# Optimization experiments

Measured on AMD Instinct MI355X. Metric: run time of the kernel, lower is better.

## Reference

```python
import jax, jax.numpy as jnp
import numpy as np

DIM = 256
NH = 8
HD = DIM // NH          # 32
KD = HD // 2            # 16, attn_ratio=0.5
SCALE = KD ** -0.5
EPS = 1e-3              # BatchNorm2d eps=0.001
B, H, W = 8, 32, 32


def _bn(x, g, b, m, v):
    # inference-mode BatchNorm2d over channel axis 1 of NCHW
    inv = g / jnp.sqrt(v + EPS)
    return x * inv[None, :, None, None] + (b - m * inv)[None, :, None, None]


def setup_inputs() -> dict:
    key = jax.random.key(0)
    ks = jax.random.split(key, 16)
    h_out = DIM + 2 * NH * KD  # 512
    return {
        "x": jax.random.normal(ks[0], (B, DIM, H, W), jnp.float32),
        "qkv_w": jax.random.normal(ks[1], (h_out, DIM), jnp.float32) * 0.05,
        "qkv_g": jax.random.uniform(ks[2], (h_out,), jnp.float32, 0.5, 1.5),
        "qkv_b": jax.random.normal(ks[3], (h_out,), jnp.float32) * 0.1,
        "qkv_m": jax.random.normal(ks[4], (h_out,), jnp.float32) * 0.1,
        "qkv_v": jax.random.uniform(ks[5], (h_out,), jnp.float32, 0.5, 1.5),
        "pe_w": jax.random.normal(ks[6], (DIM, 1, 3, 3), jnp.float32) * 0.1,
        "pe_g": jax.random.uniform(ks[7], (DIM,), jnp.float32, 0.5, 1.5),
        "pe_b": jax.random.normal(ks[8], (DIM,), jnp.float32) * 0.1,
        "pe_m": jax.random.normal(ks[9], (DIM,), jnp.float32) * 0.1,
        "pe_v": jax.random.uniform(ks[10], (DIM,), jnp.float32, 0.5, 1.5),
        "proj_w": jax.random.normal(ks[11], (DIM, DIM), jnp.float32) * 0.05,
        "proj_g": jax.random.uniform(ks[12], (DIM,), jnp.float32, 0.5, 1.5),
        "proj_b": jax.random.normal(ks[13], (DIM,), jnp.float32) * 0.1,
        "proj_m": jax.random.normal(ks[14], (DIM,), jnp.float32) * 0.1,
        "proj_v": jax.random.uniform(ks[15], (DIM,), jnp.float32, 0.5, 1.5),
    }


def reference(x, qkv_w, qkv_g, qkv_b, qkv_m, qkv_v,
              pe_w, pe_g, pe_b, pe_m, pe_v,
              proj_w, proj_g, proj_b, proj_m, proj_v):
    b, c, h, w = x.shape
    n = h * w
    # qkv: 1x1 conv (no bias) + BN, act=Identity
    qkv = _bn(jnp.einsum('oc,bchw->bohw', qkv_w, x), qkv_g, qkv_b, qkv_m, qkv_v)
    qkv = qkv.reshape(b, NH, 2 * KD + HD, n)
    q, k, v = jnp.split(qkv, [KD, 2 * KD], axis=2)  # [b,nh,kd,n],[b,nh,kd,n],[b,nh,hd,n]
    # attn = q^T @ k * scale, softmax over keys (last dim)
    attn = jax.nn.softmax(jnp.einsum('bhkn,bhkm->bhnm', q, k) * SCALE, axis=-1)
    # v @ attn^T -> [b,nh,hd,n]
    out = jnp.einsum('bhdj,bhij->bhdi', v, attn).reshape(b, c, h, w)
    # depthwise 3x3 positional branch on v (reshaped to spatial)
    v_sp = v.reshape(b, c, h, w)
    pe = jax.lax.conv_general_dilated(v_sp, pe_w, window_strides=(1, 1),
                                      padding=((1, 1), (1, 1)),
                                      feature_group_count=c)
    pe = _bn(pe, pe_g, pe_b, pe_m, pe_v)
    x_attn = out + pe
    # final 1x1 projection + BN
    return _bn(jnp.einsum('oc,bchw->bohw', proj_w, x_attn),
               proj_g, proj_b, proj_m, proj_v)
```

## Files before the change

### kernel.cpp

```cpp
#include <hip/hip_runtime.h>
#include <hip/hip_bf16.h>

#define B_    8
#define DIM_  256
#define NH_   8
#define HD_   32
#define KD_   16
#define HOUT_ 512
#define N_    1024
#define SCALE_ 0.25f
#define EPS_  1e-3f

typedef unsigned short u16;
typedef unsigned int   u32;
typedef __attribute__((ext_vector_type(8)))  short short8;
typedef __attribute__((ext_vector_type(4)))  float f32x4;
typedef __attribute__((ext_vector_type(16))) float f32x16;

union H4 { uint2 u; u16 e[4]; };
union FragU { uint4 u; short8 s; };
union F8 { short8 s; u16 e[8]; };

__device__ __forceinline__ float b2f(u16 u) {
    union { unsigned int i; float f; } c;
    c.i = ((unsigned int)u) << 16;
    return c.f;
}

__device__ __forceinline__ u16 f2b(float f) {
    union { float f; unsigned int i; } c;
    c.f = f;
    unsigned int x = c.i;
    return (u16)((x + 0x7fffu + ((x >> 16) & 1u)) >> 16);
}

__device__ __forceinline__ short8 cvt8(const float* p) {
    float4 a = ((const float4*)p)[0];
    float4 b = ((const float4*)p)[1];
    F8 f;
    f.e[0] = f2b(a.x); f.e[1] = f2b(a.y); f.e[2] = f2b(a.z); f.e[3] = f2b(a.w);
    f.e[4] = f2b(b.x); f.e[5] = f2b(b.y); f.e[6] = f2b(b.z); f.e[7] = f2b(b.w);
    return f.s;
}

__global__ __launch_bounds__(256) void k_qkv(
    const float* __restrict__ x, const float* __restrict__ qw,
    const float* __restrict__ qg, const float* __restrict__ qb,
    const float* __restrict__ qm, const float* __restrict__ qv,
    u16* __restrict__ qkv)
{
    __shared__ u16 x_s[128][40];
    __shared__ float2 bn_s[64];
    int blk = blockIdx.x;
    int nb = blk & 7, ob = (blk >> 3) & 7, b = blk >> 6;
    int t = threadIdx.x;
    int wv_ = t >> 6, lane = t & 63, quad = lane >> 4, l16 = lane & 15;
    int o_base = ob * 64 + (wv_ & 1) * 32;
    int nw = (wv_ >> 1) * 64;

    if (t < 64) {
        int o = ob * 64 + t;
        float inv  = qg[o] / sqrtf(qv[o] + EPS_);
        float beta = qb[o] - qm[o] * inv;
        if (t < 16) { inv *= SCALE_; beta *= SCALE_; }
        bn_s[t] = make_float2(inv, beta);
    }

    f32x4 acc[2][4];
    #pragma unroll
    for (int ot = 0; ot < 2; ++ot)
        #pragma unroll
        for (int nt = 0; nt < 4; ++nt) acc[ot][nt] = (f32x4){0.f, 0.f, 0.f, 0.f};

    const float* xb = x + (size_t)b * DIM_ * N_ + nb * 128;
    int sn = t & 127;
    int sc = (t >> 7) * 16;

    for (int c0 = 0; c0 < DIM_; c0 += 32) {
        short8 af[2];
        #pragma unroll
        for (int ot = 0; ot < 2; ++ot)
            af[ot] = cvt8(qw + (size_t)(o_base + ot * 16 + l16) * DIM_ + c0 + quad * 8);
        __syncthreads();
        {
            u16 tmp[16];
            #pragma unroll
            for (int j = 0; j < 16; ++j)
                tmp[j] = f2b(xb[(size_t)(c0 + sc + j) * N_ + sn]);
            *(uint4*)&x_s[sn][sc]     = *(uint4*)&tmp[0];
            *(uint4*)&x_s[sn][sc + 8] = *(uint4*)&tmp[8];
        }
        __syncthreads();
        short8 bf[4];
        #pragma unroll
        for (int nt = 0; nt < 4; ++nt)
            bf[nt] = *(const short8*)&x_s[nw + nt * 16 + l16][quad * 8];
        #pragma unroll
        for (int ot = 0; ot < 2; ++ot)
            #pragma unroll
            for (int nt = 0; nt < 4; ++nt)
                acc[ot][nt] = __builtin_amdgcn_mfma_f32_16x16x32_bf16(af[ot], bf[nt], acc[ot][nt], 0, 0, 0);
    }
    #pragma unroll
    for (int ot = 0; ot < 2; ++ot)
        #pragma unroll
        for (int r = 0; r < 4; ++r) {
            int ol = (wv_ & 1) * 32 + ot * 16 + quad * 4 + r;
            float2 ib = bn_s[ol];
            u16* dst = qkv + (size_t)(b * HOUT_ + ob * 64 + ol) * N_ + nb * 128 + nw + l16;
            #pragma unroll
            for (int nt = 0; nt < 4; ++nt)
                dst[nt * 16] = f2b(acc[ot][nt][r] * ib.x + ib.y);
        }
}

struct MainS { u16 q_t[64][24]; u16 k_t[2][256][24]; };
struct EpiS  { u16 o_acc[2][32][66]; float l_s[2][64]; float v_pe[128][33]; };
union  SmemU { MainS m; EpiS e; };

__global__ __launch_bounds__(256, 4) void k_attn(
    const u16* __restrict__ qkv, const float* __restrict__ pew,
    const float* __restrict__ eg, const float* __restrict__ eb,
    const float* __restrict__ em, const float* __restrict__ ev,
    u16* __restrict__ xattnT)
{
    __shared__ SmemU su;
    __shared__ float wpe_s[32][10];
    int blk = blockIdx.x;
    int qb = blk & 15;
    int h  = (blk >> 4) & 7;
    int b  = blk >> 7;
    int t    = threadIdx.x;
    int wv_  = t >> 6;
    int lane = t & 63;
    int q5   = lane & 31;
    int hw   = lane >> 5;
    int kh   = wv_ >> 1;
    int qt   = wv_ & 1;
    const u16* base = qkv + (size_t)(b * HOUT_ + h * 64) * N_;
    int q0g = qb * 64;

    if (t < 32) {
        int c = h * 32 + t;
        float inv = eg[c] / sqrtf(ev[c] + EPS_);
        #pragma unroll
        for (int k = 0; k < 9; ++k) wpe_s[t][k] = pew[c * 9 + k] * inv;
        wpe_s[t][9] = eb[c] - em[c] * inv;
    }
    {
        int q = t & 63, d4 = (t >> 6) * 4;
        H4 hh;
        #pragma unroll
        for (int i = 0; i < 4; ++i)
            hh.e[i] = base[(size_t)(d4 + i) * N_ + q0g + q];
        *(uint2*)&su.m.q_t[q][d4] = hh.u;
    }
    __syncthreads();

    short8 qf = *(const short8*)&su.m.q_t[qt * 32 + q5][hw * 8];

    f32x16 oacc = {0.f,0.f,0.f,0.f, 0.f,0.f,0.f,0.f, 0.f,0.f,0.f,0.f, 0.f,0.f,0.f,0.f};
    float l_lane = 0.f;

    for (int ch = 0; ch < 2; ++ch) {
        __syncthreads();
        {
            #pragma unroll
            for (int s2 = 0; s2 < 2; ++s2) {
                int key = s2 * 512 + ch * 256 + t;
                #pragma unroll
                for (int d4 = 0; d4 < 16; d4 += 4) {
                    H4 hh;
                    #pragma unroll
                    for (int i = 0; i < 4; ++i)
                        hh.e[i] = base[(size_t)(16 + d4 + i) * N_ + key];
                    *(uint2*)&su.m.k_t[s2][t][d4] = hh.u;
                }
            }
        }
        __syncthreads();

        #pragma unroll 2
        for (int tile = 0; tile < 8; ++tile) {
            int key0 = kh * 512 + ch * 256 + tile * 32;
            short8 kf = *(const short8*)&su.m.k_t[kh][tile * 32 + q5][hw * 8];
            f32x16 z = {0.f,0.f,0.f,0.f, 0.f,0.f,0.f,0.f, 0.f,0.f,0.f,0.f, 0.f,0.f,0.f,0.f};
            f32x16 sT = __builtin_amdgcn_mfma_f32_32x32x16_bf16(kf, qf, z, 0, 0, 0);
            u32 pk[8];
            #pragma unroll
            for (int j = 0; j < 8; ++j) {
                float p0 = __expf(fminf(sT[2 * j], 80.f));
                float p1 = __expf(fminf(sT[2 * j + 1], 80.f));
                l_lane += p0 + p1;
                pk[j] = (u32)f2b(p0) | ((u32)f2b(p1) << 16);
            }
            #pragma unroll
            for (int s = 0; s < 2; ++s) {
                u32 s0 = hw ? pk[4 * s + 0] : pk[4 * s + 2];
                u32 s1 = hw ? pk[4 * s + 1] : pk[4 * s + 3];
                u32 r0 = __shfl_xor(s0, 32);
                u32 r1 = __shfl_xor(s1, 32);
                FragU pf;
                pf.u.x = hw ? r0 : pk[4 * s + 0];
                pf.u.y = hw ? r1 : pk[4 * s + 1];
                pf.u.z = hw ? pk[4 * s + 2] : r0;
                pf.u.w = hw ? pk[4 * s + 3] : r1;
                const u16* vsrc = base + (size_t)(32 + q5) * N_ + key0 + s * 16 + hw * 8;
                short8 vf = *(const short8*)vsrc;
                oacc = __builtin_amdgcn_mfma_f32_32x32x16_bf16(vf, pf.s, oacc, 0, 0, 0);
            }
        }
    }

    float l_q = l_lane + __shfl_xor(l_lane, 32);
    __syncthreads();

    {
        int qg = qt * 32 + q5;
        #pragma unroll
        for (int r = 0; r < 16; ++r) {
            int d = (r & 3) + 8 * (r >> 2) + 4 * hw;
            su.e.o_acc[kh][d][qg] = f2b(oacc[r]);
        }
        if (hw == 0) su.e.l_s[kh][qg] = l_q;
    }
    {
        int ybase = qb * 2 - 1;
        #pragma unroll
        for (int i = 0; i < 16; ++i) {
            int idx = i * 256 + t;
            int d = idx >> 7, px = idx & 127;
            int y = ybase + (px >> 5);
            float v = 0.f;
            if (y >= 0 && y < 32)
                v = b2f(base[(size_t)(32 + d) * N_ + y * 32 + (px & 31)]);
            su.e.v_pe[px][d] = v;
        }
    }
    __syncthreads();

    {
        int d = t & 31, pxg = t >> 5;
        float w9[9];
        #pragma unroll
        for (int k = 0; k < 9; ++k) w9[k] = wpe_s[d][k];
        float beta = wpe_s[d][9];
        int c = h * 32 + d;
        #pragma unroll
        for (int ii = 0; ii < 8; ++ii) {
            int pl = pxg * 8 + ii;
            int xx0 = pl & 31;
            float s = beta;
            #pragma unroll
            for (int dy = -1; dy <= 1; ++dy) {
                #pragma unroll
                for (int dx = -1; dx <= 1; ++dx) {
                    int xx = xx0 + dx;
                    if (xx < 0 || xx > 31) continue;
                    s += w9[(dy + 1) * 3 + (dx + 1)] * su.e.v_pe[pl + 32 + dy * 32 + dx][d];
                }
            }
            float o = b2f(su.e.o_acc[0][d][pl]) + b2f(su.e.o_acc[1][d][pl]);
            float l = su.e.l_s[0][pl] + su.e.l_s[1][pl];
            xattnT[(size_t)(b * N_ + q0g + pl) * DIM_ + c] = f2b(o / fmaxf(l, 1e-30f) + s);
        }
    }
}

__global__ __launch_bounds__(256) void k_proj(
    const u16* __restrict__ xattnT, const float* __restrict__ pw,
    const float* __restrict__ pg, const float* __restrict__ pb,
    const float* __restrict__ pm, const float* __restrict__ pv,
    float* __restrict__ out)
{
    __shared__ float2 bn_s[64];
    int blk = blockIdx.x;
    int nb = blk & 15, ob = (blk >> 4) & 3, b = blk >> 6;
    int t = threadIdx.x;
    int wv_ = t >> 6, lane = t & 63, quad = lane >> 4, l16 = lane & 15;
    int o_base = ob * 64 + (wv_ & 1) * 32;
    int n_base = nb * 64 + (wv_ >> 1) * 32;

    if (t < 64) {
        int o = ob * 64 + t;
        float inv = pg[o] / sqrtf(pv[o] + EPS_);
        bn_s[t] = make_float2(inv, pb[o] - pm[o] * inv);
    }
    __syncthreads();

    f32x4 acc[2][2];
    #pragma unroll
    for (int ot = 0; ot < 2; ++ot)
        #pragma unroll
        for (int nt = 0; nt < 2; ++nt) acc[ot][nt] = (f32x4){0.f, 0.f, 0.f, 0.f};

    const u16* xb = xattnT + (size_t)b * N_ * DIM_;
    for (int c0 = 0; c0 < DIM_; c0 += 32) {
        short8 af[2];
        #pragma unroll
        for (int ot = 0; ot < 2; ++ot)
            af[ot] = cvt8(pw + (size_t)(o_base + ot * 16 + l16) * DIM_ + c0 + quad * 8);
        short8 bf[2];
        #pragma unroll
        for (int nt = 0; nt < 2; ++nt)
            bf[nt] = *(const short8*)(xb + (size_t)(n_base + nt * 16 + l16) * DIM_ + c0 + quad * 8);
        #pragma unroll
        for (int ot = 0; ot < 2; ++ot)
            #pragma unroll
            for (int nt = 0; nt < 2; ++nt)
                acc[ot][nt] = __builtin_amdgcn_mfma_f32_16x16x32_bf16(af[ot], bf[nt], acc[ot][nt], 0, 0, 0);
    }
    #pragma unroll
    for (int ot = 0; ot < 2; ++ot)
        #pragma unroll
        for (int r = 0; r < 4; ++r) {
            int ol = (wv_ & 1) * 32 + ot * 16 + quad * 4 + r;
            float2 ib = bn_s[ol];
            float* dst = out + (size_t)(b * DIM_ + ob * 64 + ol) * N_ + n_base + l16;
            #pragma unroll
            for (int nt = 0; nt < 2; ++nt)
                dst[nt * 16] = acc[ot][nt][r] * ib.x + ib.y;
        }
}

extern "C" void kernel_launch(void* const* d_in, const int* in_sizes, int n_in,
                              void* d_out, int out_size, void* d_ws, size_t ws_size,
                              hipStream_t stream)
{
    const float* x      = (const float*)d_in[0];
    const float* qkv_w  = (const float*)d_in[1];
    const float* qkv_g  = (const float*)d_in[2];
    const float* qkv_b  = (const float*)d_in[3];
    const float* qkv_m  = (const float*)d_in[4];
    const float* qkv_v  = (const float*)d_in[5];
    const float* pe_w   = (const float*)d_in[6];
    const float* pe_g   = (const float*)d_in[7];
    const float* pe_b   = (const float*)d_in[8];
    const float* pe_m   = (const float*)d_in[9];
    const float* pe_v   = (const float*)d_in[10];
    const float* proj_w = (const float*)d_in[11];
    const float* proj_g = (const float*)d_in[12];
    const float* proj_b = (const float*)d_in[13];
    const float* proj_m = (const float*)d_in[14];
    const float* proj_v = (const float*)d_in[15];
    float* out = (float*)d_out;

    char* p = (char*)d_ws;
    u16* qkv    = (u16*)p;  p += (size_t)B_ * HOUT_ * N_ * sizeof(u16);
    u16* xattnT = (u16*)p;

    hipLaunchKernelGGL(k_qkv, dim3(512), dim3(256), 0, stream,
                       x, qkv_w, qkv_g, qkv_b, qkv_m, qkv_v, qkv);
    hipLaunchKernelGGL(k_attn, dim3(1024), dim3(256), 0, stream,
                       qkv, pe_w, pe_g, pe_b, pe_m, pe_v, xattnT);
    hipLaunchKernelGGL(k_proj, dim3(512), dim3(256), 0, stream,
                       xattnT, proj_w, proj_g, proj_b, proj_m, proj_v, out);
}
```

Measured before the change: 146.8 us.

## Give each attention wave all keys for its own query tile, halving the grid

Each attention block now handles 128 queries, and each of its four waves processes all 1024 keys for its own 32 queries. Before, waves split the keys in half and the two partial results were merged through shared memory. The full K for the head is staged once into shared memory, split into lo/hi halves with padded rows, so the per-chunk reload and extra barriers go away. The 1/l normalisation is applied in registers before the epilogue. Risks: half as many blocks (512), a larger shared-memory footprint, and the occupancy hint removed, which may lower occupancy and latency hiding.

```diff
diff --git a/kernel.cpp b/kernel.cpp
--- a/kernel.cpp
+++ b/kernel.cpp
@@ -20,6 +20,7 @@
 union H4 { uint2 u; u16 e[4]; };
 union FragU { uint4 u; short8 s; };
 union F8 { short8 s; u16 e[8]; };
+union F8u { uint2 u2[2]; short8 s; };
 
 __device__ __forceinline__ float b2f(u16 u) {
     union { unsigned int i; float f; } c;
@@ -114,11 +115,11 @@
         }
 }
 
-struct MainS { u16 q_t[64][24]; u16 k_t[2][256][24]; };
-struct EpiS  { u16 o_acc[2][32][66]; float l_s[2][64]; float v_pe[128][33]; };
+struct MainS { u16 q_lo[128][10]; u16 q_hi[128][10]; u16 k_lo[1024][10]; u16 k_hi[1024][10]; };
+struct EpiS  { float v_pe[192][33]; u16 o_s[4][32][34]; };
 union  SmemU { MainS m; EpiS e; };
 
-__global__ __launch_bounds__(256, 4) void k_attn(
+__global__ __launch_bounds__(256) void k_attn(
     const u16* __restrict__ qkv, const float* __restrict__ pew,
     const float* __restrict__ eg, const float* __restrict__ eb,
     const float* __restrict__ em, const float* __restrict__ ev,
@@ -127,18 +128,16 @@
     __shared__ SmemU su;
     __shared__ float wpe_s[32][10];
     int blk = blockIdx.x;
-    int qb = blk & 15;
-    int h  = (blk >> 4) & 7;
-    int b  = blk >> 7;
+    int qb = blk & 7;
+    int h  = (blk >> 3) & 7;
+    int b  = blk >> 6;
     int t    = threadIdx.x;
     int wv_  = t >> 6;
     int lane = t & 63;
     int q5   = lane & 31;
     int hw   = lane >> 5;
-    int kh   = wv_ >> 1;
-    int qt   = wv_ & 1;
     const u16* base = qkv + (size_t)(b * HOUT_ + h * 64) * N_;
-    int q0g = qb * 64;
+    int q0g = qb * 128;
 
     if (t < 32) {
         int c = h * 32 + t;
@@ -148,93 +147,102 @@
         wpe_s[t][9] = eb[c] - em[c] * inv;
     }
     {
-        int q = t & 63, d4 = (t >> 6) * 4;
-        H4 hh;
-        #pragma unroll
-        for (int i = 0; i < 4; ++i)
-            hh.e[i] = base[(size_t)(d4 + i) * N_ + q0g + q];
-        *(uint2*)&su.m.q_t[q][d4] = hh.u;
+        int q = t & 127, half = t >> 7;
+        u16 tmp[8];
+        #pragma unroll
+        for (int j = 0; j < 8; ++j)
+            tmp[j] = base[(size_t)(half * 8 + j) * N_ + q0g + q];
+        u16 (*dst)[10] = half ? su.m.q_hi : su.m.q_lo;
+        *(uint2*)&dst[q][0] = *(uint2*)&tmp[0];
+        *(uint2*)&dst[q][4] = *(uint2*)&tmp[4];
+    }
+    {
+        #pragma unroll
+        for (int s = 0; s < 4; ++s) {
+            int key = s * 256 + t;
+            u16 tmp[16];
+            #pragma unroll
+            for (int d = 0; d < 16; ++d)
+                tmp[d] = base[(size_t)(16 + d) * N_ + key];
+            *(uint2*)&su.m.k_lo[key][0] = *(uint2*)&tmp[0];
+            *(uint2*)&su.m.k_lo[key][4] = *(uint2*)&tmp[4];
+            *(uint2*)&su.m.k_hi[key][0] = *(uint2*)&tmp[8];
+            *(uint2*)&su.m.k_hi[key][4] = *(uint2*)&tmp[12];
+        }
     }
     __syncthreads();
 
-    short8 qf = *(const short8*)&su.m.q_t[qt * 32 + q5][hw * 8];
+    const u16 (*qarr)[10] = hw ? su.m.q_hi : su.m.q_lo;
+    const u16 (*karr)[10] = hw ? su.m.k_hi : su.m.k_lo;
+    short8 qf;
+    {
+        F8u f;
+        f.u2[0] = *(const uint2*)&qarr[wv_ * 32 + q5][0];
+        f.u2[1] = *(const uint2*)&qarr[wv_ * 32 + q5][4];
+        qf = f.s;
+    }
 
     f32x16 oacc = {0.f,0.f,0.f,0.f, 0.f,0.f,0.f,0.f, 0.f,0.f,0.f,0.f, 0.f,0.f,0.f,0.f};
     float l_lane = 0.f;
 
-    for (int ch = 0; ch < 2; ++ch) {
-        __syncthreads();
-        {
-            #pragma unroll
-            for (int s2 = 0; s2 < 2; ++s2) {
-                int key = s2 * 512 + ch * 256 + t;
-                #pragma unroll
-                for (int d4 = 0; d4 < 16; d4 += 4) {
-                    H4 hh;
-                    #pragma unroll
-                    for (int i = 0; i < 4; ++i)
-                        hh.e[i] = base[(size_t)(16 + d4 + i) * N_ + key];
-                    *(uint2*)&su.m.k_t[s2][t][d4] = hh.u;
-                }
-            }
-        }
-        __syncthreads();
-
-        #pragma unroll 2
-        for (int tile = 0; tile < 8; ++tile) {
-            int key0 = kh * 512 + ch * 256 + tile * 32;
-            short8 kf = *(const short8*)&su.m.k_t[kh][tile * 32 + q5][hw * 8];
-            f32x16 z = {0.f,0.f,0.f,0.f, 0.f,0.f,0.f,0.f, 0.f,0.f,0.f,0.f, 0.f,0.f,0.f,0.f};
-            f32x16 sT = __builtin_amdgcn_mfma_f32_32x32x16_bf16(kf, qf, z, 0, 0, 0);
-            u32 pk[8];
-            #pragma unroll
-            for (int j = 0; j < 8; ++j) {
-                float p0 = __expf(fminf(sT[2 * j], 80.f));
-                float p1 = __expf(fminf(sT[2 * j + 1], 80.f));
-                l_lane += p0 + p1;
-                pk[j] = (u32)f2b(p0) | ((u32)f2b(p1) << 16);
-            }
-            #pragma unroll
-            for (int s = 0; s < 2; ++s) {
-                u32 s0 = hw ? pk[4 * s + 0] : pk[4 * s + 2];
-                u32 s1 = hw ? pk[4 * s + 1] : pk[4 * s + 3];
-                u32 r0 = __shfl_xor(s0, 32);
-                u32 r1 = __shfl_xor(s1, 32);
-                FragU pf;
-                pf.u.x = hw ? r0 : pk[4 * s + 0];
-                pf.u.y = hw ? r1 : pk[4 * s + 1];
-                pf.u.z = hw ? pk[4 * s + 2] : r0;
-                pf.u.w = hw ? pk[4 * s + 3] : r1;
-                const u16* vsrc = base + (size_t)(32 + q5) * N_ + key0 + s * 16 + hw * 8;
-                short8 vf = *(const short8*)vsrc;
-                oacc = __builtin_amdgcn_mfma_f32_32x32x16_bf16(vf, pf.s, oacc, 0, 0, 0);
-            }
+    #pragma unroll 4
+    for (int tile = 0; tile < 32; ++tile) {
+        int key0 = tile * 32;
+        F8u kfu;
+        kfu.u2[0] = *(const uint2*)&karr[key0 + q5][0];
+        kfu.u2[1] = *(const uint2*)&karr[key0 + q5][4];
+        f32x16 z = {0.f,0.f,0.f,0.f, 0.f,0.f,0.f,0.f, 0.f,0.f,0.f,0.f, 0.f,0.f,0.f,0.f};
+        f32x16 sT = __builtin_amdgcn_mfma_f32_32x32x16_bf16(kfu.s, qf, z, 0, 0, 0);
+        u32 pk[8];
+        #pragma unroll
+        for (int j = 0; j < 8; ++j) {
+            float p0 = __expf(fminf(sT[2 * j], 80.f));
+            float p1 = __expf(fminf(sT[2 * j + 1], 80.f));
+            l_lane += p0 + p1;
+            pk[j] = (u32)f2b(p0) | ((u32)f2b(p1) << 16);
+        }
+        #pragma unroll
+        for (int s = 0; s < 2; ++s) {
+            u32 s0 = hw ? pk[4 * s + 0] : pk[4 * s + 2];
+            u32 s1 = hw ? pk[4 * s + 1] : pk[4 * s + 3];
+            u32 r0 = __shfl_xor(s0, 32);
+            u32 r1 = __shfl_xor(s1, 32);
+            FragU pf;
+            pf.u.x = hw ? r0 : pk[4 * s + 0];
+            pf.u.y = hw ? r1 : pk[4 * s + 1];
+            pf.u.z = hw ? pk[4 * s + 2] : r0;
+            pf.u.w = hw ? pk[4 * s + 3] : r1;
+            const u16* vsrc = base + (size_t)(32 + q5) * N_ + key0 + s * 16 + hw * 8;
+            short8 vf = *(const short8*)vsrc;
+            oacc = __builtin_amdgcn_mfma_f32_32x32x16_bf16(vf, pf.s, oacc, 0, 0, 0);
         }
     }
 
     float l_q = l_lane + __shfl_xor(l_lane, 32);
+    float linv = 1.f / fmaxf(l_q, 1e-30f);
     __syncthreads();
 
     {
-        int qg = qt * 32 + q5;
         #pragma unroll
         for (int r = 0; r < 16; ++r) {
             int d = (r & 3) + 8 * (r >> 2) + 4 * hw;
-            su.e.o_acc[kh][d][qg] = f2b(oacc[r]);
-        }
-        if (hw == 0) su.e.l_s[kh][qg] = l_q;
-    }
-    {
-        int ybase = qb * 2 - 1;
-        #pragma unroll
-        for (int i = 0; i < 16; ++i) {
-            int idx = i * 256 + t;
-            int d = idx >> 7, px = idx & 127;
-            int y = ybase + (px >> 5);
-            float v = 0.f;
-            if (y >= 0 && y < 32)
-                v = b2f(base[(size_t)(32 + d) * N_ + y * 32 + (px & 31)]);
-            su.e.v_pe[px][d] = v;
+            su.e.o_s[wv_][d][q5] = f2b(oacc[r] * linv);
+        }
+    }
+    {
+        int ybase = qb * 4 - 1;
+        int px = t & 31, dg = t >> 5;
+        #pragma unroll
+        for (int j = 0; j < 6; ++j) {
+            int y = ybase + j;
+            #pragma unroll
+            for (int s = 0; s < 4; ++s) {
+                int d = dg + s * 8;
+                float v = 0.f;
+                if (y >= 0 && y < 32)
+                    v = b2f(base[(size_t)(32 + d) * N_ + y * 32 + px]);
+                su.e.v_pe[j * 32 + px][d] = v;
+            }
         }
     }
     __syncthreads();
@@ -247,8 +255,8 @@
         float beta = wpe_s[d][9];
         int c = h * 32 + d;
         #pragma unroll
-        for (int ii = 0; ii < 8; ++ii) {
-            int pl = pxg * 8 + ii;
+        for (int ii = 0; ii < 16; ++ii) {
+            int pl = pxg * 16 + ii;
             int xx0 = pl & 31;
             float s = beta;
             #pragma unroll
@@ -260,9 +268,8 @@
                     s += w9[(dy + 1) * 3 + (dx + 1)] * su.e.v_pe[pl + 32 + dy * 32 + dx][d];
                 }
             }
-            float o = b2f(su.e.o_acc[0][d][pl]) + b2f(su.e.o_acc[1][d][pl]);
-            float l = su.e.l_s[0][pl] + su.e.l_s[1][pl];
-            xattnT[(size_t)(b * N_ + q0g + pl) * DIM_ + c] = f2b(o / fmaxf(l, 1e-30f) + s);
+            float o = b2f(su.e.o_s[pl >> 5][d][pl & 31]);
+            xattnT[(size_t)(b * N_ + q0g + pl) * DIM_ + c] = f2b(o + s);
         }
     }
 }
@@ -351,7 +358,7 @@
 
     hipLaunchKernelGGL(k_qkv, dim3(512), dim3(256), 0, stream,
                        x, qkv_w, qkv_g, qkv_b, qkv_m, qkv_v, qkv);
-    hipLaunchKernelGGL(k_attn, dim3(1024), dim3(256), 0, stream,
+    hipLaunchKernelGGL(k_attn, dim3(512), dim3(256), 0, stream,
                        qkv, pe_w, pe_g, pe_b, pe_m, pe_v, xattnT);
     hipLaunchKernelGGL(k_proj, dim3(512), dim3(256), 0, stream,
                        xattnT, proj_w, proj_g, proj_b, proj_m, proj_v, out);
```

New measurement: 156.5 us. 6.6% more time.
